# Performance work log

Measured on AMD Instinct MI355X. Metric: run time of the kernel, lower is better.

The kernel has to match this reference:

```python
import jax, jax.numpy as jnp
import numpy as np

N6 = 100000
N8 = 100000
E = 400000
D = 128


def setup_inputs() -> dict:
    key = jax.random.key(0)
    ks = jax.random.split(key, 12)
    def msg(k):
        return jax.random.normal(k, (E, D), dtype=jnp.float32)
    def W(k):
        return jax.random.normal(k, (D, D), dtype=jnp.float32) / np.sqrt(D)
    def ei(k, n):
        return jax.random.randint(k, (E, 2), 0, n, dtype=jnp.int32)
    return {
        "msg_66": msg(ks[0]), "msg_68": msg(ks[1]),
        "msg_86": msg(ks[2]), "msg_88": msg(ks[3]),
        "W_66": W(ks[4]), "W_68": W(ks[5]), "W_86": W(ks[6]), "W_88": W(ks[7]),
        "ei_66": ei(ks[8], N6), "ei_68": ei(ks[9], N8),
        "ei_86": ei(ks[10], N6), "ei_88": ei(ks[11], N8),
        "num_nodes_6": N6, "num_nodes_8": N8,
    }


def _scatter_mean(v, dst, num_nodes):
    # torch_scatter reduce='mean': sum / count, count clamped to >=1 (zeros stay zero)
    s = jax.ops.segment_sum(v, dst, num_segments=num_nodes)
    c = jax.ops.segment_sum(jnp.ones((dst.shape[0],), v.dtype), dst, num_segments=num_nodes)
    return s / jnp.maximum(c, 1.0)[:, None]


def _proj_scatter(msg, W, ei, num_nodes):
    # per-edge-type linear (bias=False) then scatter-mean to dst nodes
    out = _scatter_mean(msg @ W, ei[:, 1], num_nodes)          # (num_nodes, D)
    # non-zero-row indicator (computed on detached values in the original)
    mask = jnp.any(jax.lax.stop_gradient(out) != 0, axis=-1).astype(out.dtype)  # (num_nodes,)
    return out, mask


def reference(msg_66, msg_68, msg_86, msg_88,
              W_66, W_68, W_86, W_88,
              ei_66, ei_68, ei_86, ei_88,
              num_nodes_6, num_nodes_8):
    # dict iteration order: "6-6", "6-8", "8-6", "8-8"; dst type is last token of key
    o66, m66 = _proj_scatter(msg_66, W_66, ei_66, num_nodes_6)
    o68, m68 = _proj_scatter(msg_68, W_68, ei_68, num_nodes_8)
    o86, m86 = _proj_scatter(msg_86, W_86, ei_86, num_nodes_6)
    o88, m88 = _proj_scatter(msg_88, W_88, ei_88, num_nodes_8)
    out_6 = jnp.stack([o66, o86], axis=1)   # (N6, num_edge_types_to_6=2, D)
    out_8 = jnp.stack([o68, o88], axis=1)   # (N8, 2, D)
    num_types_6 = m66 + m86                 # (N6,)
    num_types_8 = m68 + m88                 # (N8,)
    return out_6, out_8, num_types_6, num_types_8
```

## Files before the change

### kernel.cpp

```cpp
#include <hip/hip_runtime.h>

#define DF    128
#define EPB   1024
#define MAXB  512
#define TPB   64
#define CAP   640

typedef __attribute__((ext_vector_type(8))) short short8;
typedef __attribute__((ext_vector_type(4))) float f32x4;
typedef __attribute__((ext_vector_type(2))) float f32x2;

__device__ __forceinline__ unsigned short f2bf(float x) {
    unsigned u = __float_as_uint(x);
    u = (u + 0x7FFFu + ((u >> 16) & 1u)) >> 16;
    return (unsigned short)u;
}
__device__ __forceinline__ unsigned pack2bf(float a, float b) {
    return (unsigned)f2bf(a) | ((unsigned)f2bf(b) << 16);
}
__device__ __forceinline__ int rfl(int x) {
    return __builtin_amdgcn_readfirstlane(x);
}

struct AllParams {
    const float* msg[4];
    const float* Wm[4];
    float*       outp[4];
    float*       ntp[4];
    int ogb[4];
    int gb[4];
    int eb[4];
    int N[4];
    int tcnt[4];
    int cumB[5];
};


__global__ void __launch_bounds__(256) count_kernel(
    const int* __restrict__ ei66, const int* __restrict__ ei86,
    const int* __restrict__ ei68, const int* __restrict__ ei88,
    int E66, int E86, int E68, int E88, int N6, int N8,
    int* __restrict__ base)
{
    int Etot = E66 + E86 + E68 + E88;
    for (int gid = blockIdx.x * 256 + threadIdx.x; gid < Etot;
         gid += gridDim.x * 256) {
        int le = gid, nb, dst;
        if (le < E66)               { dst = ei66[2 * le + 1]; nb = 0; }
        else if ((le -= E66) < E86) { dst = ei86[2 * le + 1]; nb = N6; }
        else if ((le -= E86) < E68) { dst = ei68[2 * le + 1]; nb = 2 * N6; }
        else { le -= E68;             dst = ei88[2 * le + 1]; nb = 2 * N6 + N8; }
        atomicAdd(base + nb + dst, 1);
    }
}

__global__ void __launch_bounds__(256) scan1_kernel(
    int* __restrict__ data, int M, int* __restrict__ bsum)
{
    __shared__ int ts[256];
    int t = threadIdx.x;
    int i0 = blockIdx.x * EPB + t * 4;
    int v0 = 0, v1 = 0, v2 = 0, v3 = 0;
    if (i0 + 3 < M) {
        int4 q = *(const int4*)(data + i0);
        v0 = q.x; v1 = q.y; v2 = q.z; v3 = q.w;
    } else {
        if (i0     < M) v0 = data[i0];
        if (i0 + 1 < M) v1 = data[i0 + 1];
        if (i0 + 2 < M) v2 = data[i0 + 2];
    }
    int sum = v0 + v1 + v2 + v3;
    ts[t] = sum;
    __syncthreads();
    for (int off = 1; off < 256; off <<= 1) {
        int x = (t >= off) ? ts[t - off] : 0;
        __syncthreads();
        ts[t] += x;
        __syncthreads();
    }
    int excl = ts[t] - sum;
    if (t == 255) bsum[blockIdx.x] = ts[255];
    int w0 = excl, w1 = excl + v0, w2 = w1 + v1, w3 = w2 + v2;
    if (i0 + 3 < M) {
        *(int4*)(data + i0) = make_int4(w0, w1, w2, w3);
    } else {
        if (i0     < M) data[i0]     = w0;
        if (i0 + 1 < M) data[i0 + 1] = w1;
        if (i0 + 2 < M) data[i0 + 2] = w2;
    }
}

__global__ void __launch_bounds__(256) scan2_kernel(int* __restrict__ bsum, int nb)
{
    __shared__ int s[MAXB];
    int t = threadIdx.x;
    s[t]       = (t       < nb) ? bsum[t]       : 0;
    s[t + 256] = (t + 256 < nb) ? bsum[t + 256] : 0;
    __syncthreads();
    int o0 = s[t], o1 = s[t + 256];
    for (int off = 1; off < MAXB; off <<= 1) {
        int a = (t       >= off) ? s[t       - off] : 0;
        int b = (t + 256 >= off) ? s[t + 256 - off] : 0;
        __syncthreads();
        s[t] += a; s[t + 256] += b;
        __syncthreads();
    }
    if (t       < nb) bsum[t]       = s[t]       - o0;
    if (t + 256 < nb) bsum[t + 256] = s[t + 256] - o1;
}

__global__ void __launch_bounds__(256) scan3_kernel(
    int* __restrict__ data, int M, const int* __restrict__ bsum)
{
    int add = bsum[blockIdx.x];
    if (add == 0) return;
    int i0 = blockIdx.x * EPB + threadIdx.x * 4;
    if (i0 + 3 < M) {
        int4 q = *(const int4*)(data + i0);
        q.x += add; q.y += add; q.z += add; q.w += add;
        *(int4*)(data + i0) = q;
    } else {
        if (i0     < M) data[i0]     += add;
        if (i0 + 1 < M) data[i0 + 1] += add;
        if (i0 + 2 < M) data[i0 + 2] += add;
    }
}

__global__ void __launch_bounds__(256) fill_kernel(
    const int* __restrict__ ei66, const int* __restrict__ ei86,
    const int* __restrict__ ei68, const int* __restrict__ ei88,
    int E66, int E86, int E68, int E88, int N6, int N8,
    int* __restrict__ base, int* __restrict__ csr)
{
    int Etot = E66 + E86 + E68 + E88;
    for (int gid = blockIdx.x * 256 + threadIdx.x; gid < Etot;
         gid += gridDim.x * 256) {
        int le = gid, nb, dst;
        if (le < E66)               { dst = ei66[2 * le + 1]; nb = 0; }
        else if ((le -= E66) < E86) { dst = ei86[2 * le + 1]; nb = N6; }
        else if ((le -= E86) < E68) { dst = ei68[2 * le + 1]; nb = 2 * N6; }
        else { le -= E68;             dst = ei88[2 * le + 1]; nb = 2 * N6 + N8; }
        int pos = atomicAdd(base + nb + dst, 1);
        csr[pos] = (int)((unsigned)gid | (((unsigned)(dst & 63)) << 26));
    }
}

__global__ void __launch_bounds__(512, 4) gather_mfma_kernel(
    const int* __restrict__ base, const int* __restrict__ csr, AllParams P)
{
    __shared__ alignas(16) short Wt[DF * DF];
    __shared__ alignas(16) short At[8][16 * DF];
    __shared__ int eids[2][CAP];
    __shared__ int ends_s[2][TPB + 1];

    const int t    = threadIdx.x;
    const int lane = t & 63;
    const int w    = t >> 6;
    const int hf   = w >> 2;
    const int tl   = t & 255;
    const int wl   = w & 3;
    const int l15  = lane & 15;
    const int lg   = lane >> 4;
    short* Atw = At[w];

    const int bb = blockIdx.x;
    const int ty = (bb >= P.cumB[2]) ? ((bb >= P.cumB[3]) ? 3 : 2)
                                     : ((bb >= P.cumB[1]) ? 1 : 0);
    const float* msg = P.msg[ty];
    const int gbase = P.gb[ty], ebase = P.eb[ty], N = P.N[ty];
    const int tile  = (bb - P.cumB[ty]) * 2 + hf;
    const bool act  = (tile < P.tcnt[ty]);
    const int n0    = tile * TPB;

    {
        const float* Wm = P.Wm[ty];
        for (int idx = t; idx < 2048; idx += 512) {
            int k0 = (idx >> 5) << 1;
            int ng = (idx & 31) << 2;
            float4 wa = *(const float4*)(Wm + (size_t)k0 * DF + ng);
            float4 wb = *(const float4*)(Wm + (size_t)(k0 + 1) * DF + ng);
            float wav[4] = {wa.x, wa.y, wa.z, wa.w};
            float wbv[4] = {wb.x, wb.y, wb.z, wb.w};
            int cb = k0 >> 3, kl = k0 & 7;
            #pragma unroll
            for (int j = 0; j < 4; ++j) {
                int n = ng + j;
                int chunk = cb ^ (n & 7);
                *(unsigned*)(Wt + n * DF + chunk * 8 + kl) =
                    pack2bf(wav[j], wbv[j]);
            }
        }
    }

    if (tl <= TPB) {
        int v = 0;
        if (act) {
            int nn = n0 + tl - 1;
            if (nn >= N) nn = N - 1;
            int gi = gbase + nn;
            v = (gi >= 0) ? base[gi] : 0;
        }
        ends_s[hf][tl] = v;
    }
    if (act) {
        int gi0   = gbase + n0 - 1;
        int myts0 = (gi0 >= 0) ? base[gi0] : 0;
        int nn = n0 + TPB - 1; if (nn >= N) nn = N - 1;
        int myts1 = base[gbase + nn];
        int tot_all = myts1 - myts0;
        for (int i = tl; i < tot_all && i < CAP; i += 256)
            eids[hf][i] = csr[myts0 + i];
    }
    __syncthreads();

    const int ts0   = ends_s[hf][0];
    const int wrow0 = wl * 16;
    const int s0    = ends_s[hf][wrow0];
    const int s1    = ends_s[hf][wrow0 + 16];
    const int lbase = s0 - ts0;
    const int tot   = s1 - s0;
    int   cur = wrow0;
    float ax = 0.f, ay = 0.f;

#define FLUSHR() {                                                            \
    int lr_ = cur & 15;                                                       \
    *(unsigned*)(Atw + lr_ * DF + ((((lane >> 2) ^ (lr_ & 7))) << 3)          \
                 + ((lane & 3) << 1)) = pack2bf(ax, ay);                      \
    ax = 0.f; ay = 0.f; ++cur; }

#define CONSB(vX, rwX, sb) { _Pragma("unroll")                                \
    for (int j = 0; j < 8; ++j) {                                             \
        if ((sb) + j < tot) {                                                 \
            int rl = wrow0 + ((rwX >> (4*j)) & 15);                           \
            while (cur < rl) FLUSHR();                                        \
            ax += vX[j][0]; ay += vX[j][1]; } } }

#define ISSUE(vX, rwX, sb) {                                                  \
    rwX = 0;                                                                  \
    _Pragma("unroll")                                                         \
    for (int j = 0; j < 8; ++j) {                                             \
        int ls = (sb) + j; ls = (ls < tot) ? ls : (tot - 1);                  \
        unsigned ee = (unsigned)rfl(eids[hf][lbase + ls]);                    \
        rwX |= (int)((((ee >> 26) & 63u) - (unsigned)wrow0) & 15u) << (4*j);  \
        const float* ap = msg + (size_t)((int)(ee & 0x03FFFFFFu) - ebase) * DF \
                          + 2 * lane;                                         \
        asm volatile("global_load_dwordx2 %0, %1, off"                        \
                     : "=v"(vX[j]) : "v"(ap)); } }

#define WAITC(n) { asm volatile("s_waitcnt vmcnt(" #n ")");                   \
    __builtin_amdgcn_sched_barrier(0); }

    if (tot > 0) {
        if (lbase + tot <= CAP) {
            f32x2 v0[8], v1[8], v2[8], v3[8];
            int rw0, rw1, rw2, rw3;
            ISSUE(v0, rw0, 0)
            ISSUE(v1, rw1, 8)
            ISSUE(v2, rw2, 16)
            ISSUE(v3, rw3, 24)
            const int nb = (tot + 7) >> 3;
            int ib = 0;
            while (true) {
                WAITC(24) CONSB(v0, rw0, ib * 8)
                if (++ib >= nb) break;
                ISSUE(v0, rw0, ib * 8 + 24)
                WAITC(24) CONSB(v1, rw1, ib * 8)
                if (++ib >= nb) break;
                ISSUE(v1, rw1, ib * 8 + 24)
                WAITC(24) CONSB(v2, rw2, ib * 8)
                if (++ib >= nb) break;
                ISSUE(v2, rw2, ib * 8 + 24)
                WAITC(24) CONSB(v3, rw3, ib * 8)
                if (++ib >= nb) break;
                ISSUE(v3, rw3, ib * 8 + 24)
            }
            WAITC(0)
        } else {
            f32x2 vv[8];
            int rw;
            const int nb = (tot + 7) >> 3;
            for (int ib = 0; ib < nb; ++ib) {
                rw = 0;
                #pragma unroll
                for (int j = 0; j < 8; ++j) {
                    int ls = ib * 8 + j; ls = (ls < tot) ? ls : (tot - 1);
                    int gs = lbase + ls;
                    unsigned ee = (unsigned)rfl(
                        (gs < CAP) ? eids[hf][gs] : csr[ts0 + gs]);
                    rw |= (int)((((ee >> 26) & 63u) - (unsigned)wrow0) & 15u)
                          << (4 * j);
                    const float* ap = msg
                        + (size_t)((int)(ee & 0x03FFFFFFu) - ebase) * DF
                        + 2 * lane;
                    vv[j] = *(const f32x2*)ap;
                }
                CONSB(vv, rw, ib * 8)
            }
        }
    }
    while (cur < wrow0 + 16) FLUSHR();
#undef FLUSHR
#undef CONSB
#undef ISSUE
#undef WAITC

    f32x4 acc[8];
    #pragma unroll
    for (int j = 0; j < 8; ++j) acc[j] = (f32x4){0.f, 0.f, 0.f, 0.f};

    #pragma unroll
    for (int kk = 0; kk < 4; ++kk) {
        int c = kk * 4 + lg;
        short8 av = *(const short8*)(Atw + l15 * DF + ((c ^ (l15 & 7)) << 3));
        #pragma unroll
        for (int j = 0; j < 8; ++j) {
            int n = j * 16 + l15;
            short8 bv = *(const short8*)(Wt + n * DF + ((c ^ (n & 7)) << 3));
            acc[j] = __builtin_amdgcn_mfma_f32_16x16x32_bf16(
                av, bv, acc[j], 0, 0, 0);
        }
    }

    #pragma unroll
    for (int q = 0; q < 4; ++q) {
        int lrow = wl * 16 + lg * 4 + q;
        int dg = ends_s[hf][lrow + 1] - ends_s[hf][lrow];
        float inv = (dg > 0) ? (1.0f / (float)dg) : 0.0f;
        #pragma unroll
        for (int j = 0; j < 8; ++j) acc[j][q] *= inv;
    }

    float* fA = (float*)Atw;
    float* outp = P.outp[ty];
    #pragma unroll
    for (int h = 0; h < 2; ++h) {
        if ((lg >> 1) == h) {
            int lr = (lg & 1) << 2;
            #pragma unroll
            for (int q = 0; q < 4; ++q)
                #pragma unroll
                for (int j = 0; j < 8; ++j)
                    fA[(lr + q) * DF + j * 16 + l15] = acc[j][q];
        }
        asm volatile("" ::: "memory");
        #pragma unroll
        for (int rr = 0; rr < 4; ++rr) {
            int lrh  = 2 * rr + (lane >> 5);
            int node = n0 + wl * 16 + 8 * h + lrh;
            float4 x = *(const float4*)(fA + lrh * DF + (lane & 31) * 4);
            if (act && node < N)
                *(float4*)(outp + (size_t)node * 256 + (lane & 31) * 4) = x;
        }
        asm volatile("" ::: "memory");
    }

    float* ntp = P.ntp[ty];
    if (ntp && act && tl < TPB) {
        int nn = n0 + tl;
        if (nn < N) {
            int g_o  = P.ogb[ty] + nn;
            int st_o = (g_o > 0) ? base[g_o - 1] : 0;
            int d_o  = base[g_o] - st_o;
            int d_m  = ends_s[hf][tl + 1] - ends_s[hf][tl];
            ntp[nn] = (float)((d_o > 0) + (d_m > 0));
        }
    }
}

extern "C" void kernel_launch(void* const* d_in, const int* in_sizes, int n_in,
                              void* d_out, int out_size, void* d_ws, size_t ws_size,
                              hipStream_t stream)
{
    const float* msg66 = (const float*)d_in[0];
    const float* msg68 = (const float*)d_in[1];
    const float* msg86 = (const float*)d_in[2];
    const float* msg88 = (const float*)d_in[3];
    const float* W66   = (const float*)d_in[4];
    const float* W68   = (const float*)d_in[5];
    const float* W86   = (const float*)d_in[6];
    const float* W88   = (const float*)d_in[7];
    const int*   ei66  = (const int*)d_in[8];
    const int*   ei68  = (const int*)d_in[9];
    const int*   ei86  = (const int*)d_in[10];
    const int*   ei88  = (const int*)d_in[11];

    int E66 = in_sizes[8]  / 2;
    int E68 = in_sizes[9]  / 2;
    int E86 = in_sizes[10] / 2;
    int E88 = in_sizes[11] / 2;
    int Etot = E66 + E86 + E68 + E88;

    size_t S  = (size_t)out_size / 257;
    int    N6 = (int)(S / 2);
    int    N8 = (int)(S - S / 2);
    int    M  = 2 * N6 + 2 * N8;

    float* out  = (float*)d_out;
    float* out6 = out;
    float* out8 = out + (size_t)N6 * 256;
    float* nt6  = out + (size_t)(N6 + N8) * 256;
    float* nt8  = nt6 + N6;

    int* base = (int*)d_ws;
    int* bsum = base + M;
    int* csr  = bsum + MAXB;

    int NB = (M + EPB - 1) / EPB;

    hipMemsetAsync(base, 0, (size_t)M * sizeof(int), stream);

    int eg = (Etot + 255) / 256;
    if (eg > 4096) eg = 4096;
    count_kernel<<<dim3(eg), dim3(256), 0, stream>>>(
        ei66, ei86, ei68, ei88, E66, E86, E68, E88, N6, N8, base);

    scan1_kernel<<<dim3(NB), dim3(256), 0, stream>>>(base, M, bsum);
    scan2_kernel<<<dim3(1),  dim3(256), 0, stream>>>(bsum, NB);
    scan3_kernel<<<dim3(NB), dim3(256), 0, stream>>>(base, M, bsum);

    fill_kernel<<<dim3(eg), dim3(256), 0, stream>>>(
        ei66, ei86, ei68, ei88, E66, E86, E68, E88, N6, N8, base, csr);

    int t6 = (N6 + TPB - 1) / TPB, t8 = (N8 + TPB - 1) / TPB;
    int b6 = (t6 + 1) / 2,        b8 = (t8 + 1) / 2;
    AllParams P;
    P.msg[0] = msg66; P.Wm[0] = W66; P.outp[0] = out6;       P.gb[0] = 0;           P.eb[0] = 0;                P.N[0] = N6; P.tcnt[0] = t6;
    P.msg[1] = msg86; P.Wm[1] = W86; P.outp[1] = out6 + 128; P.gb[1] = N6;          P.eb[1] = E66;              P.N[1] = N6; P.tcnt[1] = t6;
    P.msg[2] = msg68; P.Wm[2] = W68; P.outp[2] = out8;       P.gb[2] = 2 * N6;      P.eb[2] = E66 + E86;        P.N[2] = N8; P.tcnt[2] = t8;
    P.msg[3] = msg88; P.Wm[3] = W88; P.outp[3] = out8 + 128; P.gb[3] = 2 * N6 + N8; P.eb[3] = E66 + E86 + E68;  P.N[3] = N8; P.tcnt[3] = t8;
    P.ntp[0] = nullptr; P.ogb[0] = 0;
    P.ntp[1] = nt6;     P.ogb[1] = 0;
    P.ntp[2] = nullptr; P.ogb[2] = 0;
    P.ntp[3] = nt8;     P.ogb[3] = 2 * N6;
    P.cumB[0] = 0;
    P.cumB[1] = b6;
    P.cumB[2] = 2 * b6;
    P.cumB[3] = 2 * b6 + b8;
    P.cumB[4] = 2 * b6 + 2 * b8;

    gather_mfma_kernel<<<dim3(P.cumB[4]), dim3(512), 0, stream>>>(base, csr, P);
}
```

Measured before the change: 427.8 us.

## Fuse CSR build (memset, count, scan, fill) into one cooperative kernel

Replaces the memset plus five separate launches (count, three scan phases, fill) with a single cooperative kernel of 1024 blocks that uses grid-wide syncs between phases. This removes per-launch overhead and the gaps between kernels in the preprocessing stage. In exchange it adds five grid barriers, depends on all 1024 blocks being co-resident, and gives up the wider grid (up to 4096 blocks) the atomic count and fill passes used before.

After: 889.6 us. 108% more time.

```diff
diff --git a/kernel.cpp b/kernel.cpp
--- a/kernel.cpp
+++ b/kernel.cpp
@@ -1,10 +1,12 @@
 #include <hip/hip_runtime.h>
+#include <hip/hip_cooperative_groups.h>
 
 #define DF    128
 #define EPB   1024
 #define MAXB  512
 #define TPB   64
 #define CAP   640
+#define BG    1024
 
 typedef __attribute__((ext_vector_type(8))) short short8;
 typedef __attribute__((ext_vector_type(4))) float f32x4;
@@ -35,16 +37,27 @@
     int cumB[5];
 };
 
-
-__global__ void __launch_bounds__(256) count_kernel(
+__global__ void __launch_bounds__(256) build_kernel(
     const int* __restrict__ ei66, const int* __restrict__ ei86,
     const int* __restrict__ ei68, const int* __restrict__ ei88,
     int E66, int E86, int E68, int E88, int N6, int N8,
-    int* __restrict__ base)
+    int M, int NB, int* __restrict__ base, int* __restrict__ bsum,
+    int* __restrict__ csr)
 {
-    int Etot = E66 + E86 + E68 + E88;
-    for (int gid = blockIdx.x * 256 + threadIdx.x; gid < Etot;
-         gid += gridDim.x * 256) {
+    namespace cg = cooperative_groups;
+    cg::grid_group grid = cg::this_grid();
+    __shared__ int ts[MAXB];
+
+    const int t    = threadIdx.x;
+    const int b    = blockIdx.x;
+    const int nthr = gridDim.x * 256;
+    const int g0   = b * 256 + t;
+    const int Etot = E66 + E86 + E68 + E88;
+
+    for (int i = g0; i < M; i += nthr) base[i] = 0;
+    grid.sync();
+
+    for (int gid = g0; gid < Etot; gid += nthr) {
         int le = gid, nb, dst;
         if (le < E66)               { dst = ei66[2 * le + 1]; nb = 0; }
         else if ((le -= E66) < E86) { dst = ei86[2 * le + 1]; nb = N6; }
@@ -52,89 +65,76 @@
         else { le -= E68;             dst = ei88[2 * le + 1]; nb = 2 * N6 + N8; }
         atomicAdd(base + nb + dst, 1);
     }
-}
-
-__global__ void __launch_bounds__(256) scan1_kernel(
-    int* __restrict__ data, int M, int* __restrict__ bsum)
-{
-    __shared__ int ts[256];
-    int t = threadIdx.x;
-    int i0 = blockIdx.x * EPB + t * 4;
-    int v0 = 0, v1 = 0, v2 = 0, v3 = 0;
-    if (i0 + 3 < M) {
-        int4 q = *(const int4*)(data + i0);
-        v0 = q.x; v1 = q.y; v2 = q.z; v3 = q.w;
-    } else {
-        if (i0     < M) v0 = data[i0];
-        if (i0 + 1 < M) v1 = data[i0 + 1];
-        if (i0 + 2 < M) v2 = data[i0 + 2];
-    }
-    int sum = v0 + v1 + v2 + v3;
-    ts[t] = sum;
-    __syncthreads();
-    for (int off = 1; off < 256; off <<= 1) {
-        int x = (t >= off) ? ts[t - off] : 0;
+    grid.sync();
+
+    if (b < NB) {
+        int i0 = b * EPB + t * 4;
+        int v0 = 0, v1 = 0, v2 = 0, v3 = 0;
+        if (i0 + 3 < M) {
+            int4 q = *(const int4*)(base + i0);
+            v0 = q.x; v1 = q.y; v2 = q.z; v3 = q.w;
+        } else {
+            if (i0     < M) v0 = base[i0];
+            if (i0 + 1 < M) v1 = base[i0 + 1];
+            if (i0 + 2 < M) v2 = base[i0 + 2];
+        }
+        int sum = v0 + v1 + v2 + v3;
+        ts[t] = sum;
         __syncthreads();
-        ts[t] += x;
+        for (int off = 1; off < 256; off <<= 1) {
+            int x = (t >= off) ? ts[t - off] : 0;
+            __syncthreads();
+            ts[t] += x;
+            __syncthreads();
+        }
+        int excl = ts[t] - sum;
+        if (t == 255) bsum[b] = ts[255];
+        int w0 = excl, w1 = w0 + v0, w2 = w1 + v1, w3 = w2 + v2;
+        if (i0 + 3 < M) {
+            *(int4*)(base + i0) = make_int4(w0, w1, w2, w3);
+        } else {
+            if (i0     < M) base[i0]     = w0;
+            if (i0 + 1 < M) base[i0 + 1] = w1;
+            if (i0 + 2 < M) base[i0 + 2] = w2;
+        }
+    }
+    grid.sync();
+
+    if (b == 0) {
+        ts[t]       = (t       < NB) ? bsum[t]       : 0;
+        ts[t + 256] = (t + 256 < NB) ? bsum[t + 256] : 0;
         __syncthreads();
-    }
-    int excl = ts[t] - sum;
-    if (t == 255) bsum[blockIdx.x] = ts[255];
-    int w0 = excl, w1 = excl + v0, w2 = w1 + v1, w3 = w2 + v2;
-    if (i0 + 3 < M) {
-        *(int4*)(data + i0) = make_int4(w0, w1, w2, w3);
-    } else {
-        if (i0     < M) data[i0]     = w0;
-        if (i0 + 1 < M) data[i0 + 1] = w1;
-        if (i0 + 2 < M) data[i0 + 2] = w2;
-    }
-}
-
-__global__ void __launch_bounds__(256) scan2_kernel(int* __restrict__ bsum, int nb)
-{
-    __shared__ int s[MAXB];
-    int t = threadIdx.x;
-    s[t]       = (t       < nb) ? bsum[t]       : 0;
-    s[t + 256] = (t + 256 < nb) ? bsum[t + 256] : 0;
-    __syncthreads();
-    int o0 = s[t], o1 = s[t + 256];
-    for (int off = 1; off < MAXB; off <<= 1) {
-        int a = (t       >= off) ? s[t       - off] : 0;
-        int b = (t + 256 >= off) ? s[t + 256 - off] : 0;
-        __syncthreads();
-        s[t] += a; s[t + 256] += b;
-        __syncthreads();
-    }
-    if (t       < nb) bsum[t]       = s[t]       - o0;
-    if (t + 256 < nb) bsum[t + 256] = s[t + 256] - o1;
-}
-
-__global__ void __launch_bounds__(256) scan3_kernel(
-    int* __restrict__ data, int M, const int* __restrict__ bsum)
-{
-    int add = bsum[blockIdx.x];
-    if (add == 0) return;
-    int i0 = blockIdx.x * EPB + threadIdx.x * 4;
-    if (i0 + 3 < M) {
-        int4 q = *(const int4*)(data + i0);
-        q.x += add; q.y += add; q.z += add; q.w += add;
-        *(int4*)(data + i0) = q;
-    } else {
-        if (i0     < M) data[i0]     += add;
-        if (i0 + 1 < M) data[i0 + 1] += add;
-        if (i0 + 2 < M) data[i0 + 2] += add;
-    }
-}
-
-__global__ void __launch_bounds__(256) fill_kernel(
-    const int* __restrict__ ei66, const int* __restrict__ ei86,
-    const int* __restrict__ ei68, const int* __restrict__ ei88,
-    int E66, int E86, int E68, int E88, int N6, int N8,
-    int* __restrict__ base, int* __restrict__ csr)
-{
-    int Etot = E66 + E86 + E68 + E88;
-    for (int gid = blockIdx.x * 256 + threadIdx.x; gid < Etot;
-         gid += gridDim.x * 256) {
+        int o0 = ts[t], o1 = ts[t + 256];
+        for (int off = 1; off < MAXB; off <<= 1) {
+            int a  = (t       >= off) ? ts[t       - off] : 0;
+            int b2 = (t + 256 >= off) ? ts[t + 256 - off] : 0;
+            __syncthreads();
+            ts[t] += a; ts[t + 256] += b2;
+            __syncthreads();
+        }
+        if (t       < NB) bsum[t]       = ts[t]       - o0;
+        if (t + 256 < NB) bsum[t + 256] = ts[t + 256] - o1;
+    }
+    grid.sync();
+
+    if (b < NB) {
+        int add = bsum[b];
+        if (add != 0) {
+            int i0 = b * EPB + t * 4;
+            if (i0 + 3 < M) {
+                int4 q = *(const int4*)(base + i0);
+                q.x += add; q.y += add; q.z += add; q.w += add;
+                *(int4*)(base + i0) = q;
+            } else {
+                if (i0     < M) base[i0]     += add;
+                if (i0 + 1 < M) base[i0 + 1] += add;
+                if (i0 + 2 < M) base[i0 + 2] += add;
+            }
+        }
+    }
+    grid.sync();
+
+    for (int gid = g0; gid < Etot; gid += nthr) {
         int le = gid, nb, dst;
         if (le < E66)               { dst = ei66[2 * le + 1]; nb = 0; }
         else if ((le -= E66) < E86) { dst = ei86[2 * le + 1]; nb = N6; }
@@ -407,19 +407,16 @@
 
     int NB = (M + EPB - 1) / EPB;
 
-    hipMemsetAsync(base, 0, (size_t)M * sizeof(int), stream);
-
-    int eg = (Etot + 255) / 256;
-    if (eg > 4096) eg = 4096;
-    count_kernel<<<dim3(eg), dim3(256), 0, stream>>>(
-        ei66, ei86, ei68, ei88, E66, E86, E68, E88, N6, N8, base);
-
-    scan1_kernel<<<dim3(NB), dim3(256), 0, stream>>>(base, M, bsum);
-    scan2_kernel<<<dim3(1),  dim3(256), 0, stream>>>(bsum, NB);
-    scan3_kernel<<<dim3(NB), dim3(256), 0, stream>>>(base, M, bsum);
-
-    fill_kernel<<<dim3(eg), dim3(256), 0, stream>>>(
-        ei66, ei86, ei68, ei88, E66, E86, E68, E88, N6, N8, base, csr);
+    {
+        void* args[] = {
+            (void*)&ei66, (void*)&ei86, (void*)&ei68, (void*)&ei88,
+            (void*)&E66, (void*)&E86, (void*)&E68, (void*)&E88,
+            (void*)&N6, (void*)&N8, (void*)&M, (void*)&NB,
+            (void*)&base, (void*)&bsum, (void*)&csr
+        };
+        hipLaunchCooperativeKernel((void*)build_kernel, dim3(BG), dim3(256),
+                                   args, 0, stream);
+    }
 
     int t6 = (N6 + TPB - 1) / TPB, t8 = (N8 + TPB - 1) / TPB;
     int b6 = (t6 + 1) / 2,        b8 = (t8 + 1) / 2;
```
